# Performance work log

Hardware: AMD Instinct MI355X
Metric: run time of the kernel (lower is better)

## Reference

```python
import jax, jax.numpy as jnp
import numpy as np

N = 16384          # batch of signals
DIM_T = 256        # time steps per signal
DT = 0.01          # integration dt (intg_lev=1 -> dt_intg = dt)
NUF = 256          # num_units_feat
HID_XI = 128       # hidlayers_xi
HID_AUX = 64       # hidlayers_aux1_dec
LEN_INTG = DIM_T   # (dim_t-1)*intg_lev + 1 with intg_lev=1


def _linear_init(key, fan_in, fan_out):
    # torch nn.Linear default: U(-1/sqrt(fan_in), 1/sqrt(fan_in))
    s = 1.0 / np.sqrt(fan_in)
    kw, kb = jax.random.split(key)
    W = jax.random.uniform(kw, (fan_in, fan_out), minval=-s, maxval=s, dtype=jnp.float32)
    b = jax.random.uniform(kb, (fan_out,), minval=-s, maxval=s, dtype=jnp.float32)
    return W, b


def setup_inputs() -> dict:
    key = jax.random.key(0)
    ks = jax.random.split(key, 12)
    data = jax.random.normal(ks[0], (N, DIM_T), dtype=jnp.float32)
    omega = jax.random.normal(ks[1], (N, 1), dtype=jnp.float32)
    eps = jax.random.normal(ks[2], (N, 1), dtype=jnp.float32)
    # feature extractor (mlp branch): [dim_t+1 -> 256 -> 256], relu after both (actfun_output=True)
    W_feat1, b_feat1 = _linear_init(ks[3], DIM_T + 1, NUF)
    W_feat2, b_feat2 = _linear_init(ks[4], NUF, NUF)
    # xi mean head: MLP [256 -> 128 -> 1] then Softplus
    W_xim1, b_xim1 = _linear_init(ks[5], NUF, HID_XI)
    W_xim2, b_xim2 = _linear_init(ks[6], HID_XI, 1)
    # xi lnvar head: MLP [256 -> 128 -> 1]
    W_xil1, b_xil1 = _linear_init(ks[7], NUF, HID_XI)
    W_xil2, b_xil2 = _linear_init(ks[8], HID_XI, 1)
    # decoder aux1 MLP: [dim_z_aux1+1=2 -> 64 -> 1]
    W_aux1, b_aux1 = _linear_init(ks[9], 2, HID_AUX)
    W_aux2, b_aux2 = _linear_init(ks[10], HID_AUX, 1)
    return dict(data=data, omega=omega, eps=eps,
                W_feat1=W_feat1, b_feat1=b_feat1, W_feat2=W_feat2, b_feat2=b_feat2,
                W_xim1=W_xim1, b_xim1=b_xim1, W_xim2=W_xim2, b_xim2=b_xim2,
                W_xil1=W_xil1, b_xil1=b_xil1, W_xil2=W_xil2, b_xil2=b_xil2,
                W_aux1=W_aux1, b_aux1=b_aux1, W_aux2=W_aux2, b_aux2=b_aux2)


def reference(data, omega, eps,
              W_feat1, b_feat1, W_feat2, b_feat2,
              W_xim1, b_xim1, W_xim2, b_xim2,
              W_xil1, b_xil1, W_xil2, b_xil2,
              W_aux1, b_aux1, W_aux2, b_aux2):
    relu = jax.nn.relu
    # ---- encode_xi ----
    x_ = jnp.concatenate([data, omega], axis=1)                 # [n, dim_t+1]
    feat = relu(relu(x_ @ W_feat1 + b_feat1) @ W_feat2 + b_feat2)  # [n, 256]
    xi_mean = jax.nn.softplus(relu(feat @ W_xim1 + b_xim1) @ W_xim2 + b_xim2)  # [n, 1]
    xi_lnvar = relu(feat @ W_xil1 + b_xil1) @ W_xil2 + b_xil2                  # [n, 1]
    # ---- draw (reparameterization + clamp to feasible range [0, 1]) ----
    xi = xi_mean + jnp.exp(0.5 * xi_lnvar) * eps
    xi = jnp.clip(xi, 0.0, 1.0)
    # ---- decode: Euler odeint over LEN_INTG steps of state yy=[y, dy/dt] ----
    init_y = data[:, :1]                                        # [n, 1]
    initcond = jnp.concatenate([init_y, jnp.zeros_like(init_y)], axis=1)  # [n, 2]

    def step(yy, _):
        # physics: d[y, v]/dt = [v, 0]; aux MLP adds acceleration from (z_aux1=omega, y)
        aux_in = jnp.concatenate([omega, yy[:, :1]], axis=1)    # [n, 2]
        acc = relu(aux_in @ W_aux1 + b_aux1) @ W_aux2 + b_aux2  # [n, 1]
        dyy = jnp.concatenate([yy[:, 1:2], acc], axis=1)        # [n, 2]
        return yy + DT * dyy, yy

    _, yy_seq = jax.lax.scan(step, initcond, None, length=LEN_INTG)  # [len_intg, n, 2]
    y_seq = yy_seq[:, :, 0].T                                   # [n, dim_t] (intg_lev=1)
    t_intg = DT * jnp.arange(LEN_INTG, dtype=jnp.float32)       # [dim_t]
    x_PAB = jnp.exp(-jnp.abs(xi) * t_intg[None, :]) * y_seq     # [n, dim_t]
    return xi_mean, xi_lnvar, x_PAB
```

## Files before the change

### kernel.cpp

```cpp
#include <hip/hip_runtime.h>
#include <math.h>

#define NROWS 16384
#define DT_C 0.01f

typedef short s16x8 __attribute__((ext_vector_type(8)));
typedef float f32x4 __attribute__((ext_vector_type(4)));
typedef float f32x2 __attribute__((ext_vector_type(2)));

__device__ __forceinline__ unsigned short f2bf(float f) {
    unsigned u = __float_as_uint(f);
    u += 0x7fffu + ((u >> 16) & 1u);
    return (unsigned short)(u >> 16);
}
__device__ __forceinline__ unsigned packtr(float a, float b) {
    return __builtin_amdgcn_perm(__float_as_uint(b), __float_as_uint(a), 0x07060302u);
}
template <int CTRL>
__device__ __forceinline__ float dppadd(float v) {
    int x = __builtin_amdgcn_update_dpp(0, __float_as_int(v), CTRL, 0xF, 0xF, true);
    return v + __int_as_float(x);
}
__device__ __forceinline__ float sum8(float p) {
    p = dppadd<0xB1>(p);
    p = dppadd<0x4E>(p);
    p = dppadd<0x141>(p);
    return p;
}

__global__ __launch_bounds__(256) void prep_k(
    const float* __restrict__ Wf1, const float* __restrict__ Wf2,
    const float* __restrict__ Wm1, const float* __restrict__ Wl1,
    const float* __restrict__ bm1, const float* __restrict__ bl1,
    unsigned short* __restrict__ wpack, float* __restrict__ biasH)
{
    const int id = blockIdx.x * 256 + threadIdx.x;
    const int n  = id & 255;
    const int k8 = (id >> 8) & 31;
    const int s  = id >> 13;

    unsigned short tmp[8];
    #pragma unroll
    for (int j = 0; j < 8; ++j) {
        const int k = k8 * 8 + j;
        float v;
        if (s == 0)      v = Wf1[k * 256 + n];
        else if (s == 1) v = Wf2[k * 256 + n];
        else             v = (n < 128) ? Wm1[k * 128 + n] : Wl1[k * 128 + n - 128];
        tmp[j] = f2bf(v);
    }
    *(uint4*)&wpack[((s * 32 + k8) * 256 + n) * 8] = *(const uint4*)tmp;

    if (id < 256) biasH[id] = (id < 128) ? bm1[id] : bl1[id - 128];
}

__global__ __launch_bounds__(256, 2) void fused_k(
    const float* __restrict__ data, const float* __restrict__ omega,
    const float* __restrict__ eps_g,
    const unsigned short* __restrict__ wpack, const float* __restrict__ biasH,
    const float* __restrict__ bf1, const float* __restrict__ bf2,
    const float* __restrict__ w256g,
    const float* __restrict__ Wm2, const float* __restrict__ bm2,
    const float* __restrict__ Wl2, const float* __restrict__ bl2,
    const float* __restrict__ Wa1, const float* __restrict__ ba1,
    const float* __restrict__ Wa2, const float* __restrict__ ba2,
    float* __restrict__ out_mean, float* __restrict__ out_lnvar,
    float* __restrict__ xout)
{
    __shared__ __align__(16) unsigned char smem[33024];
    unsigned short* As1 = (unsigned short*)smem;
    unsigned short* Hs  = (unsigned short*)(smem + 16384);
    float* headsF = (float*)smem;
    float* omg = (float*)(smem + 32768);
    float* xiS = omg + 32;

    const int tid  = threadIdx.x;
    const int wid  = tid >> 6;
    const int lane = tid & 63;
    const int ln   = lane & 15;
    const int quad = lane >> 4;
    const int r0   = blockIdx.x * 32;

    {
        #pragma unroll
        for (int g2 = 0; g2 < 8; ++g2) {
            const int unit = g2 * 256 + tid;
            const int m    = unit >> 6;
            const int c16  = unit & 63;
            const int kblk = c16 >> 1;
            const int h    = c16 & 1;
            const float4 v = *(const float4*)&data[(size_t)(r0 + m) * 256 + c16 * 4];
            unsigned* d = (unsigned*)&As1[((kblk * 32) + (m ^ (kblk & 7))) * 8 + h * 4];
            d[0] = packtr(v.x, v.y);
            d[1] = packtr(v.z, v.w);
        }
        if (tid < 32) omg[tid] = omega[r0 + tid];
    }

    f32x4 acc[2][4];

    auto seed = [&](const float* bias) {
        #pragma unroll
        for (int nt = 0; nt < 4; ++nt) {
            const float b = bias[wid * 64 + nt * 16 + ln];
            acc[0][nt] = f32x4{b, b, b, b};
            acc[1][nt] = acc[0][nt];
        }
    };

    auto run_stage = [&](const unsigned short* Ap, const unsigned short* wp) {
        #pragma unroll
        for (int c = 0; c < 4; ++c) {
            #pragma unroll
            for (int kk = 0; kk < 2; ++kk) {
                const int kb   = kk * 4 + quad;
                const int kblk = c * 8 + kb;
                const int f    = kblk & 7;
                const unsigned short* bp = wp + ((size_t)(kblk * 256) + wid * 64 + ln) * 8;
                s16x8 b0 = *(const s16x8*)(bp + 0 * 128);
                s16x8 b1 = *(const s16x8*)(bp + 1 * 128);
                s16x8 b2 = *(const s16x8*)(bp + 2 * 128);
                s16x8 b3 = *(const s16x8*)(bp + 3 * 128);
                s16x8 a0 = *(const s16x8*)&Ap[(kblk * 32 + (ln ^ f)) * 8];
                s16x8 a1 = *(const s16x8*)&Ap[(kblk * 32 + ((ln ^ f) + 16)) * 8];
                acc[0][0] = __builtin_amdgcn_mfma_f32_16x16x32_bf16(a0, b0, acc[0][0], 0, 0, 0);
                acc[1][0] = __builtin_amdgcn_mfma_f32_16x16x32_bf16(a1, b0, acc[1][0], 0, 0, 0);
                acc[0][1] = __builtin_amdgcn_mfma_f32_16x16x32_bf16(a0, b1, acc[0][1], 0, 0, 0);
                acc[1][1] = __builtin_amdgcn_mfma_f32_16x16x32_bf16(a1, b1, acc[1][1], 0, 0, 0);
                acc[0][2] = __builtin_amdgcn_mfma_f32_16x16x32_bf16(a0, b2, acc[0][2], 0, 0, 0);
                acc[1][2] = __builtin_amdgcn_mfma_f32_16x16x32_bf16(a1, b2, acc[1][2], 0, 0, 0);
                acc[0][3] = __builtin_amdgcn_mfma_f32_16x16x32_bf16(a0, b3, acc[0][3], 0, 0, 0);
                acc[1][3] = __builtin_amdgcn_mfma_f32_16x16x32_bf16(a1, b3, acc[1][3], 0, 0, 0);
            }
        }
    };

    auto write_packed = [&](unsigned short* dst, bool addOm) {
        #pragma unroll
        for (int nt = 0; nt < 4; ++nt) {
            const int col = wid * 64 + nt * 16 + ln;
            const int kg  = col >> 3, f = kg & 7, jj = col & 7;
            const float wo = addOm ? w256g[col] : 0.f;
            #pragma unroll
            for (int mt = 0; mt < 2; ++mt) {
                #pragma unroll
                for (int r = 0; r < 4; ++r) {
                    const int row = mt * 16 + quad * 4 + r;
                    float v = acc[mt][nt][r];
                    if (addOm) v = fmaf(omg[row], wo, v);
                    v = fmaxf(v, 0.f);
                    dst[(kg * 32 + (row ^ f)) * 8 + jj] =
                        (unsigned short)(__float_as_uint(v) >> 16);
                }
            }
        }
    };

    __syncthreads();
    seed(bf1);
    run_stage(As1, wpack);
    write_packed(Hs, true);
    __syncthreads();
    seed(bf2);
    run_stage(Hs, wpack + 65536);
    write_packed(As1, false);
    __syncthreads();
    seed(biasH);
    run_stage(As1, wpack + 131072);
    __syncthreads();
    #pragma unroll
    for (int nt = 0; nt < 4; ++nt) {
        const int col = wid * 64 + nt * 16 + ln;
        #pragma unroll
        for (int mt = 0; mt < 2; ++mt) {
            #pragma unroll
            for (int r = 0; r < 4; ++r) {
                const int row = mt * 16 + quad * 4 + r;
                headsF[row * 256 + ((col + row * 8) & 255)] = fmaxf(acc[mt][nt][r], 0.f);
            }
        }
    }
    __syncthreads();

    {
        const int m = tid >> 3, l = tid & 7;
        float pm = 0.f, pl = 0.f;
        #pragma unroll
        for (int q = 0; q < 4; ++q) {
            const int c0 = l * 16 + q * 4;
            const float4 hm = *(const float4*)&headsF[m * 256 + ((c0 + m * 8) & 255)];
            const float4 wm = *(const float4*)&Wm2[c0];
            const float4 hl = *(const float4*)&headsF[m * 256 + ((128 + c0 + m * 8) & 255)];
            const float4 wl = *(const float4*)&Wl2[c0];
            pm = fmaf(hm.w, wm.w, fmaf(hm.z, wm.z, fmaf(hm.y, wm.y, fmaf(hm.x, wm.x, pm))));
            pl = fmaf(hl.w, wl.w, fmaf(hl.z, wl.z, fmaf(hl.y, wl.y, fmaf(hl.x, wl.x, pl))));
        }
        pm = sum8(pm);
        pl = sum8(pl);
        if (l == 0) {
            const float xm   = pm + bm2[0];
            const float mean = fmaxf(xm, 0.f) + log1pf(expf(-fabsf(xm)));
            const float lnv  = pl + bl2[0];
            out_mean[r0 + m]  = mean;
            out_lnvar[r0 + m] = lnv;
            float xi = mean + expf(0.5f * lnv) * eps_g[r0 + m];
            xiS[m] = fminf(fmaxf(xi, 0.f), 1.f);
        }
    }
    __syncthreads();

    {
        const int r   = tid >> 3;
        const int l   = tid & 7;
        const int row = r0 + r;
        const float om = omg[r];
        const float s  = __expf(-xiS[r] * DT_C);
        const float pseed = ba2[0] * 0.125f;

        f32x2 w1v[4], Av[4], w2v[4];
        #pragma unroll
        for (int i = 0; i < 4; ++i) {
            const f32x2 w0 = *(const f32x2*)&Wa1[l * 8 + i * 2];
            const f32x2 bb = *(const f32x2*)&ba1[l * 8 + i * 2];
            w1v[i] = *(const f32x2*)&Wa1[64 + l * 8 + i * 2];
            w2v[i] = *(const f32x2*)&Wa2[l * 8 + i * 2];
            Av[i]  = f32x2{fmaf(om, w0.x, bb.x), fmaf(om, w0.y, bb.y)};
        }

        auto partial = [&](float y) -> float {
            const f32x2 y2 = f32x2{y, y};
            f32x2 a0 = f32x2{pseed, 0.f};
            f32x2 a1 = f32x2{0.f, 0.f};
            #pragma unroll
            for (int i = 0; i < 4; ++i) {
                f32x2 h = __builtin_elementwise_fma(y2, w1v[i], Av[i]);
                h = __builtin_elementwise_max(h, f32x2{0.f, 0.f});
                if (i & 1) a1 = __builtin_elementwise_fma(h, w2v[i], a1);
                else       a0 = __builtin_elementwise_fma(h, w2v[i], a0);
            }
            a0 = a0 + a1;
            return a0.x + a0.y;
        };

        const float y0 = data[(size_t)row * 256];
        float ym = y0, yc = y0;
        const float DT2 = DT_C * DT_C;
        float pr = sum8(partial(ym));
        float d = 1.f;

        float* orow = xout + (size_t)row * 256 + l * 4;
        for (int tb = 0; tb < 8; ++tb) {
            float cur[4];
            #pragma unroll
            for (int j = 0; j < 32; ++j) {
                const float m_ = d * ym;
                if ((j >> 2) == l) cur[j & 3] = m_;
                d *= s;
                float pn = sum8(partial(yc));
                const float yn = fmaf(DT2, pr, fmaf(2.f, yc, -ym));
                ym = yc; yc = yn; pr = pn;
            }
            *(float4*)&orow[tb * 32] = *(const float4*)cur;
        }
    }
}

extern "C" void kernel_launch(void* const* d_in, const int* in_sizes, int n_in,
                              void* d_out, int out_size, void* d_ws, size_t ws_size,
                              hipStream_t stream)
{
    const float* data    = (const float*)d_in[0];
    const float* omega   = (const float*)d_in[1];
    const float* eps     = (const float*)d_in[2];
    const float* W_feat1 = (const float*)d_in[3];
    const float* b_feat1 = (const float*)d_in[4];
    const float* W_feat2 = (const float*)d_in[5];
    const float* b_feat2 = (const float*)d_in[6];
    const float* W_xim1  = (const float*)d_in[7];
    const float* b_xim1  = (const float*)d_in[8];
    const float* W_xim2  = (const float*)d_in[9];
    const float* b_xim2  = (const float*)d_in[10];
    const float* W_xil1  = (const float*)d_in[11];
    const float* b_xil1  = (const float*)d_in[12];
    const float* W_xil2  = (const float*)d_in[13];
    const float* b_xil2  = (const float*)d_in[14];
    const float* W_aux1  = (const float*)d_in[15];
    const float* b_aux1  = (const float*)d_in[16];
    const float* W_aux2  = (const float*)d_in[17];
    const float* b_aux2  = (const float*)d_in[18];

    float* out_mean  = (float*)d_out;
    float* out_lnvar = out_mean + NROWS;
    float* out_x     = out_lnvar + NROWS;

    unsigned short* wpack = (unsigned short*)d_ws;
    float* biasH = (float*)((char*)d_ws + 3 * 32 * 256 * 8 * 2);

    prep_k<<<96, 256, 0, stream>>>(W_feat1, W_feat2, W_xim1, W_xil1,
                                   b_xim1, b_xil1, wpack, biasH);
    fused_k<<<512, 256, 0, stream>>>(data, omega, eps, wpack, biasH,
                                     b_feat1, b_feat2, W_feat1 + 256 * 256,
                                     W_xim2, b_xim2, W_xil2, b_xil2,
                                     W_aux1, b_aux1, W_aux2, b_aux2,
                                     out_mean, out_lnvar, out_x);
}
```

Before: 142.9 us.

## Hoist B-fragment loads in MFMA stage and halve ODE threads per row

The GEMM stage now loads all weight fragments for a stage into registers before issuing the MFMAs, so global loads are batched ahead of compute. The Euler ODE phase uses 4 lanes per row (128 threads) instead of 8, each handling 16 hidden units with a shorter DPP reduction, and writes output in 16-column chunks. The softplus and reparameterization exps switch to fast __expf. Risks include higher register pressure from holding 32 B fragments, and half the threads sitting idle during the serial ODE loop.

```diff
diff --git a/kernel.cpp b/kernel.cpp
--- a/kernel.cpp
+++ b/kernel.cpp
@@ -20,6 +20,11 @@
 __device__ __forceinline__ float dppadd(float v) {
     int x = __builtin_amdgcn_update_dpp(0, __float_as_int(v), CTRL, 0xF, 0xF, true);
     return v + __int_as_float(x);
+}
+__device__ __forceinline__ float sum4(float p) {
+    p = dppadd<0xB1>(p);
+    p = dppadd<0x4E>(p);
+    return p;
 }
 __device__ __forceinline__ float sum8(float p) {
     p = dppadd<0xB1>(p);
@@ -109,28 +114,25 @@
     };
 
     auto run_stage = [&](const unsigned short* Ap, const unsigned short* wp) {
-        #pragma unroll
-        for (int c = 0; c < 4; ++c) {
-            #pragma unroll
-            for (int kk = 0; kk < 2; ++kk) {
-                const int kb   = kk * 4 + quad;
-                const int kblk = c * 8 + kb;
-                const int f    = kblk & 7;
-                const unsigned short* bp = wp + ((size_t)(kblk * 256) + wid * 64 + ln) * 8;
-                s16x8 b0 = *(const s16x8*)(bp + 0 * 128);
-                s16x8 b1 = *(const s16x8*)(bp + 1 * 128);
-                s16x8 b2 = *(const s16x8*)(bp + 2 * 128);
-                s16x8 b3 = *(const s16x8*)(bp + 3 * 128);
-                s16x8 a0 = *(const s16x8*)&Ap[(kblk * 32 + (ln ^ f)) * 8];
-                s16x8 a1 = *(const s16x8*)&Ap[(kblk * 32 + ((ln ^ f) + 16)) * 8];
-                acc[0][0] = __builtin_amdgcn_mfma_f32_16x16x32_bf16(a0, b0, acc[0][0], 0, 0, 0);
-                acc[1][0] = __builtin_amdgcn_mfma_f32_16x16x32_bf16(a1, b0, acc[1][0], 0, 0, 0);
-                acc[0][1] = __builtin_amdgcn_mfma_f32_16x16x32_bf16(a0, b1, acc[0][1], 0, 0, 0);
-                acc[1][1] = __builtin_amdgcn_mfma_f32_16x16x32_bf16(a1, b1, acc[1][1], 0, 0, 0);
-                acc[0][2] = __builtin_amdgcn_mfma_f32_16x16x32_bf16(a0, b2, acc[0][2], 0, 0, 0);
-                acc[1][2] = __builtin_amdgcn_mfma_f32_16x16x32_bf16(a1, b2, acc[1][2], 0, 0, 0);
-                acc[0][3] = __builtin_amdgcn_mfma_f32_16x16x32_bf16(a0, b3, acc[0][3], 0, 0, 0);
-                acc[1][3] = __builtin_amdgcn_mfma_f32_16x16x32_bf16(a1, b3, acc[1][3], 0, 0, 0);
+        s16x8 B[8][4];
+        #pragma unroll
+        for (int w = 0; w < 8; ++w) {
+            const int kblk = w * 4 + quad;
+            const unsigned short* bp = wp + ((size_t)(kblk * 256) + wid * 64 + ln) * 8;
+            #pragma unroll
+            for (int nt = 0; nt < 4; ++nt)
+                B[w][nt] = *(const s16x8*)(bp + nt * 128);
+        }
+        #pragma unroll
+        for (int w = 0; w < 8; ++w) {
+            const int kblk = w * 4 + quad;
+            const int f    = kblk & 7;
+            s16x8 a0 = *(const s16x8*)&Ap[(kblk * 32 + (ln ^ f)) * 8];
+            s16x8 a1 = *(const s16x8*)&Ap[(kblk * 32 + ((ln ^ f) + 16)) * 8];
+            #pragma unroll
+            for (int nt = 0; nt < 4; ++nt) {
+                acc[0][nt] = __builtin_amdgcn_mfma_f32_16x16x32_bf16(a0, B[w][nt], acc[0][nt], 0, 0, 0);
+                acc[1][nt] = __builtin_amdgcn_mfma_f32_16x16x32_bf16(a1, B[w][nt], acc[1][nt], 0, 0, 0);
             }
         }
     };
@@ -199,31 +201,32 @@
         pl = sum8(pl);
         if (l == 0) {
             const float xm   = pm + bm2[0];
-            const float mean = fmaxf(xm, 0.f) + log1pf(expf(-fabsf(xm)));
+            const float mean = fmaxf(xm, 0.f) + log1pf(__expf(-fabsf(xm)));
             const float lnv  = pl + bl2[0];
             out_mean[r0 + m]  = mean;
             out_lnvar[r0 + m] = lnv;
-            float xi = mean + expf(0.5f * lnv) * eps_g[r0 + m];
+            float xi = mean + __expf(0.5f * lnv) * eps_g[r0 + m];
             xiS[m] = fminf(fmaxf(xi, 0.f), 1.f);
         }
     }
     __syncthreads();
 
-    {
-        const int r   = tid >> 3;
-        const int l   = tid & 7;
+    if (tid < 128) {
+        const int r   = tid >> 2;
+        const int l   = tid & 3;
         const int row = r0 + r;
         const float om = omg[r];
         const float s  = __expf(-xiS[r] * DT_C);
-        const float pseed = ba2[0] * 0.125f;
-
-        f32x2 w1v[4], Av[4], w2v[4];
-        #pragma unroll
-        for (int i = 0; i < 4; ++i) {
-            const f32x2 w0 = *(const f32x2*)&Wa1[l * 8 + i * 2];
-            const f32x2 bb = *(const f32x2*)&ba1[l * 8 + i * 2];
-            w1v[i] = *(const f32x2*)&Wa1[64 + l * 8 + i * 2];
-            w2v[i] = *(const f32x2*)&Wa2[l * 8 + i * 2];
+        const float pseed = ba2[0] * 0.25f;
+
+        f32x2 w1v[8], Av[8], w2v[8];
+        #pragma unroll
+        for (int i = 0; i < 8; ++i) {
+            const int u = l * 16 + i * 2;
+            const f32x2 w0 = *(const f32x2*)&Wa1[u];
+            const f32x2 bb = *(const f32x2*)&ba1[u];
+            w1v[i] = *(const f32x2*)&Wa1[64 + u];
+            w2v[i] = *(const f32x2*)&Wa2[u];
             Av[i]  = f32x2{fmaf(om, w0.x, bb.x), fmaf(om, w0.y, bb.y)};
         }
 
@@ -231,36 +234,42 @@
             const f32x2 y2 = f32x2{y, y};
             f32x2 a0 = f32x2{pseed, 0.f};
             f32x2 a1 = f32x2{0.f, 0.f};
-            #pragma unroll
-            for (int i = 0; i < 4; ++i) {
+            f32x2 a2 = f32x2{0.f, 0.f};
+            f32x2 a3 = f32x2{0.f, 0.f};
+            #pragma unroll
+            for (int i = 0; i < 8; ++i) {
                 f32x2 h = __builtin_elementwise_fma(y2, w1v[i], Av[i]);
                 h = __builtin_elementwise_max(h, f32x2{0.f, 0.f});
-                if (i & 1) a1 = __builtin_elementwise_fma(h, w2v[i], a1);
-                else       a0 = __builtin_elementwise_fma(h, w2v[i], a0);
+                if ((i & 3) == 0) a0 = __builtin_elementwise_fma(h, w2v[i], a0);
+                if ((i & 3) == 1) a1 = __builtin_elementwise_fma(h, w2v[i], a1);
+                if ((i & 3) == 2) a2 = __builtin_elementwise_fma(h, w2v[i], a2);
+                if ((i & 3) == 3) a3 = __builtin_elementwise_fma(h, w2v[i], a3);
             }
             a0 = a0 + a1;
+            a2 = a2 + a3;
+            a0 = a0 + a2;
             return a0.x + a0.y;
         };
 
         const float y0 = data[(size_t)row * 256];
         float ym = y0, yc = y0;
         const float DT2 = DT_C * DT_C;
-        float pr = sum8(partial(ym));
+        float pr = sum4(partial(ym));
         float d = 1.f;
 
         float* orow = xout + (size_t)row * 256 + l * 4;
-        for (int tb = 0; tb < 8; ++tb) {
+        for (int b = 0; b < 16; ++b) {
             float cur[4];
             #pragma unroll
-            for (int j = 0; j < 32; ++j) {
+            for (int j = 0; j < 16; ++j) {
                 const float m_ = d * ym;
                 if ((j >> 2) == l) cur[j & 3] = m_;
                 d *= s;
-                float pn = sum8(partial(yc));
+                float pn = sum4(partial(yc));
                 const float yn = fmaf(DT2, pr, fmaf(2.f, yc, -ym));
                 ym = yc; yc = yn; pr = pn;
             }
-            *(float4*)&orow[tb * 32] = *(const float4*)cur;
+            *(float4*)&orow[b * 16] = *(const float4*)cur;
         }
     }
 }
```

Measured after the change: 156.7 us. 9.6% more time.
